# Optimization experiments

Measured on AMD Instinct MI355X. Metric: run time of the kernel, lower is better.

The kernel has to match this reference:

```python
import jax, jax.numpy as jnp
import numpy as np

BUFFER_SIZE = 64  # chunk size == sliding window size


def setup_inputs() -> dict:
    key = jax.random.key(0)
    k1, k2, k3, k4 = jax.random.split(key, 4)
    B, S, dim = 4, 8192, 256
    D = dim * 2
    states = jax.random.normal(k1, (B, S, dim, 2), dtype=jnp.float32)
    # projection weights (module inits them to identity; use scaled random for a
    # non-trivial but numerically tame reference)
    Wq = jax.random.normal(k2, (D, D), dtype=jnp.float32) * 0.05
    Wk = jax.random.normal(k3, (D, D), dtype=jnp.float32) * 0.05
    Wv = jax.random.normal(k4, (D, D), dtype=jnp.float32) * 0.05
    return {"states": states, "Wq": Wq, "Wk": Wk, "Wv": Wv}


def reference(states, Wq, Wk, Wv):
    B, S, dim, _ = states.shape
    D = dim * 2
    C = BUFFER_SIZE
    assert S % C == 0 and S > 2 * C
    n = S // C  # number of chunks

    x = states.reshape(B, S, D)
    q = x @ Wq.T
    k = x @ Wk.T
    v = x @ Wv.T

    # chunk: [B, n, C, D]
    qc = q.reshape(B, n, C, D)
    kc = k.reshape(B, n, C, D)
    vc = v.reshape(B, n, C, D)

    # context for chunk i = chunk i-1 ++ chunk i  -> [B, n, 2C, D]
    zeros_blk = jnp.zeros_like(kc[:, :1])
    k_ctx = jnp.concatenate([jnp.concatenate([zeros_blk, kc[:, :-1]], axis=1), kc], axis=2)
    v_ctx = jnp.concatenate([jnp.concatenate([zeros_blk, vc[:, :-1]], axis=1), vc], axis=2)

    scale = 1.0 / jnp.sqrt(jnp.asarray(D, dtype=q.dtype))
    scores = jnp.einsum('bnqd,bnkd->bnqk', qc, k_ctx) * scale  # [B, n, C, 2C]

    # mask: query at local pos qi attends keys strictly before it (global),
    # i.e. context index j < C + qi; chunk 0 has no previous chunk (j >= C).
    qi = jnp.arange(C)[:, None]            # [C,1]
    j = jnp.arange(2 * C)[None, :]         # [1,2C]
    chunk_idx = jnp.arange(n)[:, None, None]
    mask = (j < C + qi)[None] & ((chunk_idx > 0) | (j >= C)[None])  # [n, C, 2C]

    scores = jnp.where(mask[None], scores, jnp.asarray(-1e30, scores.dtype))
    p = jax.nn.softmax(scores, axis=-1)
    # fully-masked rows (only global position 0) -> zero output
    row_valid = jnp.any(mask, axis=-1, keepdims=True)[None].astype(p.dtype)
    p = p * row_valid

    out = jnp.einsum('bnqk,bnkd->bnqd', p, v_ctx).reshape(B, S, D)
    out = out.at[:, 0, :].set(0.0)  # matches retrieved_flat[:, 0, :] = 0.0
    return out.reshape(B, S, dim, 2)
```

## Files before the change

### kernel.cpp

```cpp
#include <hip/hip_runtime.h>

#define SCALE 0.044194173824159216f

typedef _Float16 half8 __attribute__((ext_vector_type(8)));
typedef _Float16 half4 __attribute__((ext_vector_type(4)));
typedef float    f32x4 __attribute__((ext_vector_type(4)));

#define MFMA(A, B, Cc) __builtin_amdgcn_mfma_f32_16x16x32_f16((A), (B), (Cc), 0, 0, 0)

#define X16_OFF 0ull
#define Y16_OFF 33554432ull
#define MT_OFF  67108864ull
#define MP_OFF  68157440ull
#define VT_OFF  100663296ull
#define W16_OFF 134217728ull
#define WS_NEED 135790592ull

typedef __attribute__((address_space(1))) const unsigned int glb_t;
typedef __attribute__((address_space(3))) unsigned int lds_t;

__device__ __forceinline__ void gl16(const void* g, void* l) {
  __builtin_amdgcn_global_load_lds((glb_t*)g, (lds_t*)l, 16, 0, 0);
}

__device__ __forceinline__ half8 ldf64(const _Float16* buf, int row, int colh) {
  int byte = row * 128 + (((colh) << 1) ^ ((row & 7) << 4));
  return *(const half8*)((const char*)buf + byte);
}
__device__ __forceinline__ half8 ldf128(const _Float16* buf, int row, int colh) {
  int byte = row * 256 + (((colh) << 1) ^ ((row & 7) << 4));
  return *(const half8*)((const char*)buf + byte);
}

__global__ __launch_bounds__(256)
void k0_cvt(const float* __restrict__ x, const float* __restrict__ Wq,
            const float* __restrict__ Wk, const float* __restrict__ Wv,
            _Float16* __restrict__ x16, _Float16* __restrict__ w16)
{
  const long long NX = 16777216LL;
  long long base = ((long long)blockIdx.x * 256 + threadIdx.x) * 8;
  const float* src;
  _Float16* dst;
  float sc = 1.0f;
  if (base < NX) {
    src = x + base; dst = x16 + base;
  } else {
    long long o = base - NX;
    int ws = (int)(o >> 18);
    long long oo = o & 262143LL;
    src = (ws == 0 ? Wq : (ws == 1 ? Wk : Wv)) + oo;
    dst = w16 + o;
    if (ws == 0) sc = SCALE;
  }
  const float4* p = (const float4*)src;
  float4 f0 = p[0], f1 = p[1];
  half8 v;
  v[0] = (_Float16)(f0.x * sc); v[1] = (_Float16)(f0.y * sc);
  v[2] = (_Float16)(f0.z * sc); v[3] = (_Float16)(f0.w * sc);
  v[4] = (_Float16)(f1.x * sc); v[5] = (_Float16)(f1.y * sc);
  v[6] = (_Float16)(f1.z * sc); v[7] = (_Float16)(f1.w * sc);
  *(half8*)dst = v;
}

__global__ __launch_bounds__(256)
void kmmA(const float* __restrict__ Wq, const float* __restrict__ Wk,
          float* __restrict__ part)
{
  const int blk = blockIdx.x, t = threadIdx.x;
  const int fc = blk & 7, ot = blk >> 3;
  const int G0 = (ot >> 3) * 64, E0 = (ot & 7) * 64;
  const int gb = G0 + (t & 15) * 4;
  const int eb = E0 + (t >> 4) * 4;
  float acc[4][4] = {};
  const int f0 = fc * 64;
  #pragma unroll 4
  for (int f = f0; f < f0 + 64; ++f) {
    f32x4 kv = *(const f32x4*)(Wk + (size_t)f * 512 + gb);
    f32x4 qv = *(const f32x4*)(Wq + (size_t)f * 512 + eb);
    #pragma unroll
    for (int i = 0; i < 4; ++i)
      #pragma unroll
      for (int j = 0; j < 4; ++j)
        acc[i][j] += kv[i] * qv[j];
  }
  float* pp = part + (size_t)fc * 262144;
  #pragma unroll
  for (int i = 0; i < 4; ++i)
    *(f32x4*)(pp + (size_t)(gb + i) * 512 + eb) =
        (f32x4){acc[i][0], acc[i][1], acc[i][2], acc[i][3]};
}

__global__ __launch_bounds__(256)
void kmmB(const float* __restrict__ part, _Float16* __restrict__ Mt)
{
  const int idx = blockIdx.x * 256 + threadIdx.x;
  float s = 0.f;
  #pragma unroll
  for (int fc = 0; fc < 8; ++fc)
    s += part[(size_t)fc * 262144 + idx];
  Mt[idx] = (_Float16)(s * SCALE);
}

__global__ __launch_bounds__(256)
void k1_gemm(const _Float16* __restrict__ x16, const _Float16* __restrict__ w16,
             const _Float16* __restrict__ Mt, _Float16* __restrict__ y16,
             _Float16* __restrict__ vT)
{
  __shared__ _Float16 xs[2][8192];
  __shared__ _Float16 wl[2][8192];

  const int id  = blockIdx.x;
  const int swz = (id & 7) * 256 + (id >> 3);
  const int ntile = swz & 7;
  const int stile = swz >> 3;
  const bool vpath = (ntile >= 4);
  const int tid = threadIdx.x, lane = tid & 63, w = tid >> 6;
  const int l15 = lane & 15, h = lane >> 4;
  const int wm = w >> 1, wn = w & 1;

  const _Float16* xb = x16 + (size_t)stile * 128 * 512;
  const _Float16* wb = vpath ? w16 + (size_t)(1024 + (ntile & 3) * 128) * 512
                             : Mt  + (size_t)((ntile & 3) * 128) * 512;

  int rowi[4], coli[4];
  #pragma unroll
  for (int i = 0; i < 4; ++i) {
    int unit = i * 256 + w * 64 + lane;
    int row = unit >> 3, u = unit & 7;
    rowi[i] = row;
    coli[i] = (u ^ (row & 7)) << 3;
  }

  f32x4 acc[4][4] = {};

  #pragma unroll
  for (int i = 0; i < 4; ++i) {
    int ub = i * 256 + w * 64;
    gl16(xb + (size_t)rowi[i] * 512 + coli[i], &xs[0][ub * 8]);
    gl16(wb + (size_t)rowi[i] * 512 + coli[i], &wl[0][ub * 8]);
  }

  for (int kk = 0; kk < 8; ++kk) {
    const int cur = kk & 1;
    if (kk < 7) {
      const int nxt = cur ^ 1;
      #pragma unroll
      for (int i = 0; i < 4; ++i) {
        int ub = i * 256 + w * 64;
        gl16(xb + (size_t)rowi[i] * 512 + (kk + 1) * 64 + coli[i], &xs[nxt][ub * 8]);
        gl16(wb + (size_t)rowi[i] * 512 + (kk + 1) * 64 + coli[i], &wl[nxt][ub * 8]);
      }
      asm volatile("s_waitcnt vmcnt(8)" ::: "memory");
    } else {
      asm volatile("s_waitcnt vmcnt(0)" ::: "memory");
    }
    __builtin_amdgcn_s_barrier();
    __builtin_amdgcn_sched_barrier(0);

    #pragma unroll
    for (int ks = 0; ks < 2; ++ks) {
      half8 a[4], bf[4];
      if (!vpath) {
        #pragma unroll
        for (int mr = 0; mr < 4; ++mr) a[mr]  = ldf64(xs[cur], wm * 64 + mr * 16 + l15, ks * 32 + h * 8);
        #pragma unroll
        for (int nr = 0; nr < 4; ++nr) bf[nr] = ldf64(wl[cur], wn * 64 + nr * 16 + l15, ks * 32 + h * 8);
      } else {
        #pragma unroll
        for (int mr = 0; mr < 4; ++mr) a[mr]  = ldf64(wl[cur], wm * 64 + mr * 16 + l15, ks * 32 + h * 8);
        #pragma unroll
        for (int nr = 0; nr < 4; ++nr) bf[nr] = ldf64(xs[cur], wn * 64 + nr * 16 + l15, ks * 32 + h * 8);
      }
      #pragma unroll
      for (int mr = 0; mr < 4; ++mr)
        #pragma unroll
        for (int nr = 0; nr < 4; ++nr)
          acc[mr][nr] = MFMA(a[mr], bf[nr], acc[mr][nr]);
    }

    __builtin_amdgcn_sched_barrier(0);
    __builtin_amdgcn_s_barrier();
  }

  if (!vpath) {
    const int m0 = stile * 128 + wm * 64;
    const int n0 = (ntile & 3) * 128 + wn * 64;
    #pragma unroll
    for (int mr = 0; mr < 4; ++mr)
      #pragma unroll
      for (int nr = 0; nr < 4; ++nr)
        #pragma unroll
        for (int r = 0; r < 4; ++r)
          y16[(size_t)(m0 + mr * 16 + h * 4 + r) * 512 + n0 + nr * 16 + l15] =
              (_Float16)acc[mr][nr][r];
  } else {
    const int d0 = (ntile & 3) * 128 + wm * 64;
    const int sg = stile * 128 + wn * 64;
    const int bb = sg >> 13, s0 = sg & 8191;
    _Float16* dst = vT + (size_t)bb * 512 * 8192;
    #pragma unroll
    for (int mr = 0; mr < 4; ++mr)
      #pragma unroll
      for (int nr = 0; nr < 4; ++nr)
        #pragma unroll
        for (int r = 0; r < 4; ++r)
          dst[(size_t)(d0 + mr * 16 + h * 4 + r) * 8192 + s0 + nr * 16 + l15] =
              (_Float16)acc[mr][nr][r];
  }
}

__global__ __launch_bounds__(256)
void k2_attn(const _Float16* __restrict__ y16, const _Float16* __restrict__ x16,
             const _Float16* __restrict__ vT, float* __restrict__ out)
{
  __shared__ _Float16 kj[2][128 * 64];
  __shared__ _Float16 p_lds[64 * 128];

  const int id = blockIdx.x;
  const int sz = (id & 7) * 64 + (id >> 3);
  const int b = sz >> 7, c = sz & 127;
  const int tid = threadIdx.x, lane = tid & 63, w = tid >> 6;
  const int l15 = lane & 15, h = lane >> 4;
  const int jbase = c * 64 - 64;

  const _Float16* qrow = y16 + (size_t)(b * 8192 + c * 64 + w * 16 + l15) * 512;
  half8 qa[16];
  #pragma unroll
  for (int ks = 0; ks < 16; ++ks) qa[ks] = *(const half8*)(qrow + ks * 32 + h * 8);

  const _Float16* kb = x16 + (size_t)b * 8192 * 512;
  const _Float16* vb = vT + (size_t)b * 512 * 8192;

  int srow[4], scol[4];
  #pragma unroll
  for (int i = 0; i < 4; ++i) {
    int unit = i * 256 + w * 64 + lane;
    int row = unit >> 3, u = unit & 7;
    int sj = jbase + row; if (sj < 0) sj = 0;
    srow[i] = sj;
    scol[i] = (u ^ (row & 7)) << 3;
  }
  int prow[4], pjs[4];
  #pragma unroll
  for (int i = 0; i < 4; ++i) {
    int unit = i * 256 + w * 64 + lane;
    int row = unit >> 4, u = unit & 15;
    int u2 = (u & 8) | ((u & 7) ^ (row & 7));
    int js = jbase + u2 * 8; if (js < 0) js = 0;
    prow[i] = row;
    pjs[i] = js;
  }

  f32x4 S[8] = {};
  #pragma unroll
  for (int i = 0; i < 4; ++i)
    gl16(kb + (size_t)srow[i] * 512 + scol[i], &kj[0][(i * 256 + w * 64) * 8]);

  #pragma unroll
  for (int ee = 0; ee < 8; ++ee) {
    if (ee < 7) {
      #pragma unroll
      for (int i = 0; i < 4; ++i)
        gl16(kb + (size_t)srow[i] * 512 + (ee + 1) * 64 + scol[i],
             &kj[(ee + 1) & 1][(i * 256 + w * 64) * 8]);
      asm volatile("s_waitcnt vmcnt(4)" ::: "memory");
    } else {
      asm volatile("s_waitcnt vmcnt(0)" ::: "memory");
    }
    __builtin_amdgcn_s_barrier();
    __builtin_amdgcn_sched_barrier(0);

    #pragma unroll
    for (int ks = 0; ks < 2; ++ks) {
      #pragma unroll
      for (int nt = 0; nt < 8; ++nt) {
        half8 bf = ldf64(kj[ee & 1], nt * 16 + l15, ks * 32 + h * 8);
        S[nt] = MFMA(qa[ee * 2 + ks], bf, S[nt]);
      }
    }
    __builtin_amdgcn_sched_barrier(0);
    __builtin_amdgcn_s_barrier();
  }

  #pragma unroll
  for (int i = 0; i < 4; ++i)
    gl16(vb + (size_t)prow[i] * 8192 + pjs[i], &kj[0][(i * 256 + w * 64) * 8]);

  #pragma unroll
  for (int jt = 0; jt < 8; ++jt) {
    int j = jt * 16 + l15;
    #pragma unroll
    for (int r = 0; r < 4; ++r) {
      int ql = w * 16 + h * 4 + r;
      bool valid = (j < 64 + ql) && ((c > 0) || (j >= 64));
      S[jt][r] = valid ? S[jt][r] : -1e30f;
    }
  }
  #pragma unroll
  for (int r = 0; r < 4; ++r) {
    float mx = -1e30f;
    #pragma unroll
    for (int jt = 0; jt < 8; ++jt) mx = fmaxf(mx, S[jt][r]);
    mx = fmaxf(mx, __shfl_xor(mx, 1));
    mx = fmaxf(mx, __shfl_xor(mx, 2));
    mx = fmaxf(mx, __shfl_xor(mx, 4));
    mx = fmaxf(mx, __shfl_xor(mx, 8));
    float sum = 0.f;
    #pragma unroll
    for (int jt = 0; jt < 8; ++jt) {
      float sv = S[jt][r];
      float pe = (sv > -1e29f) ? __expf(sv - mx) : 0.f;
      S[jt][r] = pe;
      sum += pe;
    }
    sum += __shfl_xor(sum, 1);
    sum += __shfl_xor(sum, 2);
    sum += __shfl_xor(sum, 4);
    sum += __shfl_xor(sum, 8);
    float inv = (sum > 0.f) ? (1.0f / sum) : 0.f;
    #pragma unroll
    for (int jt = 0; jt < 8; ++jt) {
      int row = w * 16 + h * 4 + r, col = jt * 16 + l15;
      _Float16 ph = (_Float16)(S[jt][r] * inv);
      *(_Float16*)((char*)p_lds + row * 256 + ((col << 1) ^ ((row & 7) << 4))) = ph;
    }
  }
  half8 pa[4];
  #pragma unroll
  for (int ks = 0; ks < 4; ++ks) {
    int row = w * 16 + l15, colh = ks * 32 + h * 8;
    pa[ks] = *(const half8*)((const char*)p_lds + row * 256 + ((colh << 1) ^ ((row & 7) << 4)));
  }

  float* ob = out + (size_t)(b * 8192 + c * 64 + w * 16) * 512;
  #pragma unroll
  for (int dd = 0; dd < 8; ++dd) {
    if (dd < 7) {
      #pragma unroll
      for (int i = 0; i < 4; ++i)
        gl16(vb + (size_t)((dd + 1) * 64 + prow[i]) * 8192 + pjs[i],
             &kj[(dd + 1) & 1][(i * 256 + w * 64) * 8]);
      asm volatile("s_waitcnt vmcnt(4)" ::: "memory");
    } else {
      asm volatile("s_waitcnt vmcnt(0)" ::: "memory");
    }
    __builtin_amdgcn_s_barrier();
    __builtin_amdgcn_sched_barrier(0);

    f32x4 o[4] = {};
    #pragma unroll
    for (int ks = 0; ks < 4; ++ks) {
      #pragma unroll
      for (int nr = 0; nr < 4; ++nr) {
        half8 bf = ldf128(kj[dd & 1], nr * 16 + l15, ks * 32 + h * 8);
        o[nr] = MFMA(pa[ks], bf, o[nr]);
      }
    }
    #pragma unroll
    for (int nr = 0; nr < 4; ++nr)
      #pragma unroll
      for (int r = 0; r < 4; ++r)
        ob[(size_t)(h * 4 + r) * 512 + dd * 64 + nr * 16 + l15] = o[nr][r];
    __builtin_amdgcn_sched_barrier(0);
    __builtin_amdgcn_s_barrier();
  }
}

__device__ __forceinline__ int swzb(int row, int colByte) {
  return colByte ^ ((row & 7) << 4);
}
__device__ __forceinline__ half8 ldw_frag(const float* __restrict__ W, int row, int e0) {
  const float4* p = reinterpret_cast<const float4*>(W + ((size_t)row << 9) + e0);
  float4 f0 = p[0];
  float4 f1 = p[1];
  half8 v;
  v[0] = (_Float16)f0.x; v[1] = (_Float16)f0.y; v[2] = (_Float16)f0.z; v[3] = (_Float16)f0.w;
  v[4] = (_Float16)f1.x; v[5] = (_Float16)f1.y; v[6] = (_Float16)f1.z; v[7] = (_Float16)f1.w;
  return v;
}
__device__ __forceinline__ half8 ldl_frag(const unsigned short* buf, int row, int col, int strideBytes) {
  int byte = row * strideBytes + swzb(row, col << 1);
  return *reinterpret_cast<const half8*>(reinterpret_cast<const char*>(buf) + byte);
}

__global__ __launch_bounds__(256, 1)
void ep_fused(const float* __restrict__ x, const float* __restrict__ Wq,
              const float* __restrict__ Wk, const float* __restrict__ Wv,
              float* __restrict__ out)
{
  __shared__ unsigned short xs[128 * 512];
  __shared__ unsigned short kv[64 * 128];
  __shared__ unsigned short pq[64 * 128];

  const int bc   = blockIdx.x;
  const int b    = bc >> 7;
  const int c    = bc & 127;
  const int tid  = threadIdx.x;
  const int lane = tid & 63;
  const int w    = tid >> 6;
  const int l15  = lane & 15;
  const int h    = lane >> 4;

  const float* xb = x + (size_t)b * (8192 * 512);
  #pragma unroll
  for (int i = 0; i < 32; ++i) {
    int unit = tid + (i << 8);
    int row  = unit >> 6;
    int e0   = (unit & 63) << 3;
    half8 v;
    if (c == 0 && row < 64) {
      #pragma unroll
      for (int t = 0; t < 8; ++t) v[t] = (_Float16)0.0f;
    } else {
      int s = c * 64 - 64 + row;
      const float4* p = reinterpret_cast<const float4*>(xb + (size_t)s * 512 + e0);
      float4 f0 = p[0], f1 = p[1];
      v[0] = (_Float16)f0.x; v[1] = (_Float16)f0.y; v[2] = (_Float16)f0.z; v[3] = (_Float16)f0.w;
      v[4] = (_Float16)f1.x; v[5] = (_Float16)f1.y; v[6] = (_Float16)f1.z; v[7] = (_Float16)f1.w;
    }
    int byte = (row << 10) + swzb(row, e0 << 1);
    *reinterpret_cast<half8*>(reinterpret_cast<char*>(xs) + byte) = v;
  }
  __syncthreads();

  f32x4 Sacc[8] = {};
  const int d0 = (w << 4) + (h << 2);

  for (int dt = 0; dt < 8; ++dt) {
    const int drow = (dt << 6) + (w << 4) + l15;

    f32x4 qa[4] = {};
    for (int ks = 0; ks < 16; ++ks) {
      half8 a = ldw_frag(Wq, drow, (ks << 5) + (h << 3));
      #pragma unroll
      for (int nt = 0; nt < 4; ++nt) {
        half8 bf = ldl_frag(xs, 64 + (nt << 4) + l15, (ks << 5) + (h << 3), 1024);
        qa[nt] = MFMA(a, bf, qa[nt]);
      }
    }
    #pragma unroll
    for (int nt = 0; nt < 4; ++nt) {
      int q = (nt << 4) + l15;
      half4 hv;
      hv[0] = (_Float16)qa[nt][0]; hv[1] = (_Float16)qa[nt][1];
      hv[2] = (_Float16)qa[nt][2]; hv[3] = (_Float16)qa[nt][3];
      *reinterpret_cast<half4*>(reinterpret_cast<char*>(pq) + q * 128 + swzb(q, d0 << 1)) = hv;
    }

    f32x4 ka[8] = {};
    for (int ks = 0; ks < 16; ++ks) {
      half8 a = ldw_frag(Wk, drow, (ks << 5) + (h << 3));
      #pragma unroll
      for (int nt = 0; nt < 8; ++nt) {
        half8 bf = ldl_frag(xs, (nt << 4) + l15, (ks << 5) + (h << 3), 1024);
        ka[nt] = MFMA(a, bf, ka[nt]);
      }
    }
    #pragma unroll
    for (int nt = 0; nt < 8; ++nt) {
      int j = (nt << 4) + l15;
      half4 hv;
      hv[0] = (_Float16)ka[nt][0]; hv[1] = (_Float16)ka[nt][1];
      hv[2] = (_Float16)ka[nt][2]; hv[3] = (_Float16)ka[nt][3];
      *reinterpret_cast<half4*>(reinterpret_cast<char*>(kv) + j * 128 + swzb(j, d0 << 1)) = hv;
    }
    __syncthreads();

    #pragma unroll
    for (int ksd = 0; ksd < 2; ++ksd) {
      half8 a = ldl_frag(pq, (w << 4) + l15, (ksd << 5) + (h << 3), 128);
      #pragma unroll
      for (int nt = 0; nt < 8; ++nt) {
        half8 bf = ldl_frag(kv, (nt << 4) + l15, (ksd << 5) + (h << 3), 128);
        Sacc[nt] = MFMA(a, bf, Sacc[nt]);
      }
    }
    __syncthreads();
  }

  const float scale = SCALE;
  #pragma unroll
  for (int nt = 0; nt < 8; ++nt) {
    int j = (nt << 4) + l15;
    #pragma unroll
    for (int r = 0; r < 4; ++r) {
      int qrow = (w << 4) + (h << 2) + r;
      bool valid = (j < 64 + qrow) && ((c > 0) || (j >= 64));
      Sacc[nt][r] = valid ? Sacc[nt][r] * scale : -1e30f;
    }
  }
  float inv[4];
  #pragma unroll
  for (int r = 0; r < 4; ++r) {
    float mx = -1e30f;
    #pragma unroll
    for (int nt = 0; nt < 8; ++nt) mx = fmaxf(mx, Sacc[nt][r]);
    mx = fmaxf(mx, __shfl_xor(mx, 1));
    mx = fmaxf(mx, __shfl_xor(mx, 2));
    mx = fmaxf(mx, __shfl_xor(mx, 4));
    mx = fmaxf(mx, __shfl_xor(mx, 8));
    float sum = 0.f;
    #pragma unroll
    for (int nt = 0; nt < 8; ++nt) {
      float sv = Sacc[nt][r];
      float pe = (sv > -1e29f) ? __expf(sv - mx) : 0.f;
      Sacc[nt][r] = pe;
      sum += pe;
    }
    sum += __shfl_xor(sum, 1);
    sum += __shfl_xor(sum, 2);
    sum += __shfl_xor(sum, 4);
    sum += __shfl_xor(sum, 8);
    inv[r] = (sum > 0.f) ? (1.0f / sum) : 0.f;
  }
  #pragma unroll
  for (int nt = 0; nt < 8; ++nt) {
    int j = (nt << 4) + l15;
    #pragma unroll
    for (int r = 0; r < 4; ++r) {
      int qrow = (w << 4) + (h << 2) + r;
      _Float16 ph = (_Float16)(Sacc[nt][r] * inv[r]);
      *reinterpret_cast<_Float16*>(reinterpret_cast<char*>(pq) + qrow * 256 + swzb(qrow, j << 1)) = ph;
    }
  }
  __syncthreads();

  for (int dt = 0; dt < 8; ++dt) {
    const int dcol = (dt << 6) + (w << 4) + l15;

    f32x4 va[8] = {};
    for (int ks = 0; ks < 16; ++ks) {
      half8 bf = ldw_frag(Wv, dcol, (ks << 5) + (h << 3));
      #pragma unroll
      for (int mt = 0; mt < 8; ++mt) {
        half8 a = ldl_frag(xs, (mt << 4) + l15, (ks << 5) + (h << 3), 1024);
        va[mt] = MFMA(a, bf, va[mt]);
      }
    }
    {
      int dl = (w << 4) + l15;
      #pragma unroll
      for (int mt = 0; mt < 8; ++mt) {
        int j0 = (mt << 4) + (h << 2);
        half4 hv;
        hv[0] = (_Float16)va[mt][0]; hv[1] = (_Float16)va[mt][1];
        hv[2] = (_Float16)va[mt][2]; hv[3] = (_Float16)va[mt][3];
        *reinterpret_cast<half4*>(reinterpret_cast<char*>(kv) + dl * 256 + swzb(dl, j0 << 1)) = hv;
      }
    }
    __syncthreads();

    f32x4 oa[4] = {};
    #pragma unroll
    for (int ks = 0; ks < 4; ++ks) {
      half8 a = ldl_frag(pq, (w << 4) + l15, (ks << 5) + (h << 3), 256);
      #pragma unroll
      for (int nt = 0; nt < 4; ++nt) {
        half8 bf = ldl_frag(kv, (nt << 4) + l15, (ks << 5) + (h << 3), 256);
        oa[nt] = MFMA(a, bf, oa[nt]);
      }
    }
    #pragma unroll
    for (int nt = 0; nt < 4; ++nt) {
      int d = (dt << 6) + (nt << 4) + l15;
      #pragma unroll
      for (int r = 0; r < 4; ++r) {
        int qrow = (w << 4) + (h << 2) + r;
        out[((size_t)(b * 8192 + (c << 6) + qrow) << 9) + d] = oa[nt][r];
      }
    }
    __syncthreads();
  }
}

extern "C" void kernel_launch(void* const* d_in, const int* in_sizes, int n_in,
                              void* d_out, int out_size, void* d_ws, size_t ws_size,
                              hipStream_t stream) {
  const float* x  = (const float*)d_in[0];
  const float* Wq = (const float*)d_in[1];
  const float* Wk = (const float*)d_in[2];
  const float* Wv = (const float*)d_in[3];
  float* out = (float*)d_out;
  (void)in_sizes; (void)n_in; (void)out_size;

  if (d_ws != nullptr && ws_size >= WS_NEED) {
    char* ws = (char*)d_ws;
    _Float16* x16 = (_Float16*)(ws + X16_OFF);
    _Float16* y16 = (_Float16*)(ws + Y16_OFF);
    _Float16* Mt  = (_Float16*)(ws + MT_OFF);
    float*    Mp  = (float*)(ws + MP_OFF);
    _Float16* vT  = (_Float16*)(ws + VT_OFF);
    _Float16* w16 = (_Float16*)(ws + W16_OFF);

    hipLaunchKernelGGL(kmmA, dim3(512), dim3(256), 0, stream, Wq, Wk, Mp);
    hipLaunchKernelGGL(k0_cvt, dim3(8576), dim3(256), 0, stream, x, Wq, Wk, Wv, x16, w16);
    hipLaunchKernelGGL(kmmB, dim3(1024), dim3(256), 0, stream, Mp, Mt);
    hipLaunchKernelGGL(k1_gemm, dim3(2048), dim3(256), 0, stream, x16, w16, Mt, y16, vT);
    hipLaunchKernelGGL(k2_attn, dim3(512), dim3(256), 0, stream, y16, x16, vT, out);
  } else {
    hipLaunchKernelGGL(ep_fused, dim3(512), dim3(256), 0, stream, x, Wq, Wk, Wv, out);
  }
}
```

Before: 103.7 us.

## Pre-pack weight operands into MFMA fragment layout and load them directly to registers

```diff
diff --git a/kernel.cpp b/kernel.cpp
--- a/kernel.cpp
+++ b/kernel.cpp
@@ -12,6 +12,7 @@
 #define Y16_OFF 33554432ull
 #define MT_OFF  67108864ull
 #define MP_OFF  68157440ull
+#define WF_OFF  76546048ull
 #define VT_OFF  100663296ull
 #define W16_OFF 134217728ull
 #define WS_NEED 135790592ull
@@ -91,23 +92,43 @@
 }
 
 __global__ __launch_bounds__(256)
-void kmmB(const float* __restrict__ part, _Float16* __restrict__ Mt)
+void kmmB(const float* __restrict__ part, const _Float16* __restrict__ w16,
+          _Float16* __restrict__ wfrag)
 {
-  const int idx = blockIdx.x * 256 + threadIdx.x;
-  float s = 0.f;
-  #pragma unroll
-  for (int fc = 0; fc < 8; ++fc)
-    s += part[(size_t)fc * 262144 + idx];
-  Mt[idx] = (_Float16)(s * SCALE);
+  const int T = blockIdx.x * 256 + threadIdx.x;
+  const int lane = T & 63;
+  const int rbi  = (T >> 6) & 7;
+  const int ks   = (T >> 9) & 1;
+  const int kk   = (T >> 10) & 7;
+  const int ntile = T >> 13;
+  const int gl = rbi * 16 + (lane & 15);
+  const int e0 = kk * 64 + ks * 32 + (lane >> 4) * 8;
+  half8 v;
+  if (ntile < 4) {
+    const int g = ntile * 128 + gl;
+    float s[8] = {};
+    #pragma unroll
+    for (int fc = 0; fc < 8; ++fc) {
+      const float* pp = part + (size_t)fc * 262144 + (size_t)g * 512 + e0;
+      f32x4 a = *(const f32x4*)pp;
+      f32x4 b = *(const f32x4*)(pp + 4);
+      s[0] += a[0]; s[1] += a[1]; s[2] += a[2]; s[3] += a[3];
+      s[4] += b[0]; s[5] += b[1]; s[6] += b[2]; s[7] += b[3];
+    }
+    #pragma unroll
+    for (int j = 0; j < 8; ++j) v[j] = (_Float16)(s[j] * SCALE);
+  } else {
+    const int g = (ntile - 4) * 128 + gl;
+    v = *(const half8*)(w16 + (size_t)(1024 + g) * 512 + e0);
+  }
+  *(half8*)(wfrag + (size_t)T * 8) = v;
 }
 
 __global__ __launch_bounds__(256)
-void k1_gemm(const _Float16* __restrict__ x16, const _Float16* __restrict__ w16,
-             const _Float16* __restrict__ Mt, _Float16* __restrict__ y16,
-             _Float16* __restrict__ vT)
+void k1_gemm(const _Float16* __restrict__ x16, const _Float16* __restrict__ wfrag,
+             _Float16* __restrict__ y16, _Float16* __restrict__ vT)
 {
   __shared__ _Float16 xs[2][8192];
-  __shared__ _Float16 wl[2][8192];
 
   const int id  = blockIdx.x;
   const int swz = (id & 7) * 256 + (id >> 3);
@@ -119,8 +140,8 @@
   const int wm = w >> 1, wn = w & 1;
 
   const _Float16* xb = x16 + (size_t)stile * 128 * 512;
-  const _Float16* wb = vpath ? w16 + (size_t)(1024 + (ntile & 3) * 128) * 512
-                             : Mt  + (size_t)((ntile & 3) * 128) * 512;
+  const int rbsel = vpath ? wm : wn;
+  const _Float16* wfb = wfrag + (size_t)ntile * 65536 + (size_t)rbsel * 4 * 512 + lane * 8;
 
   int rowi[4], coli[4];
   #pragma unroll
@@ -132,25 +153,31 @@
   }
 
   f32x4 acc[4][4] = {};
-
-  #pragma unroll
-  for (int i = 0; i < 4; ++i) {
-    int ub = i * 256 + w * 64;
-    gl16(xb + (size_t)rowi[i] * 512 + coli[i], &xs[0][ub * 8]);
-    gl16(wb + (size_t)rowi[i] * 512 + coli[i], &wl[0][ub * 8]);
-  }
+  half8 wf[2][8];
+
+  #pragma unroll
+  for (int i = 0; i < 4; ++i)
+    gl16(xb + (size_t)rowi[i] * 512 + coli[i], &xs[0][(i * 256 + w * 64) * 8]);
+  #pragma unroll
+  for (int f = 0; f < 4; ++f)
+    #pragma unroll
+    for (int ks = 0; ks < 2; ++ks)
+      wf[0][f * 2 + ks] = *(const half8*)(wfb + ((0 * 2 + ks) * 8 + f) * 512);
 
   for (int kk = 0; kk < 8; ++kk) {
-    const int cur = kk & 1;
+    const int cur = kk & 1, nxt = cur ^ 1;
     if (kk < 7) {
-      const int nxt = cur ^ 1;
-      #pragma unroll
-      for (int i = 0; i < 4; ++i) {
-        int ub = i * 256 + w * 64;
-        gl16(xb + (size_t)rowi[i] * 512 + (kk + 1) * 64 + coli[i], &xs[nxt][ub * 8]);
-        gl16(wb + (size_t)rowi[i] * 512 + (kk + 1) * 64 + coli[i], &wl[nxt][ub * 8]);
-      }
-      asm volatile("s_waitcnt vmcnt(8)" ::: "memory");
+      #pragma unroll
+      for (int i = 0; i < 4; ++i)
+        gl16(xb + (size_t)rowi[i] * 512 + (kk + 1) * 64 + coli[i],
+             &xs[nxt][(i * 256 + w * 64) * 8]);
+      #pragma unroll
+      for (int f = 0; f < 4; ++f)
+        #pragma unroll
+        for (int ks = 0; ks < 2; ++ks)
+          wf[nxt][f * 2 + ks] = *(const half8*)(wfb + (((kk + 1) * 2 + ks) * 8 + f) * 512);
+      __builtin_amdgcn_sched_barrier(0);
+      asm volatile("s_waitcnt vmcnt(12)" ::: "memory");
     } else {
       asm volatile("s_waitcnt vmcnt(0)" ::: "memory");
     }
@@ -159,23 +186,16 @@
 
     #pragma unroll
     for (int ks = 0; ks < 2; ++ks) {
-      half8 a[4], bf[4];
-      if (!vpath) {
-        #pragma unroll
-        for (int mr = 0; mr < 4; ++mr) a[mr]  = ldf64(xs[cur], wm * 64 + mr * 16 + l15, ks * 32 + h * 8);
-        #pragma unroll
-        for (int nr = 0; nr < 4; ++nr) bf[nr] = ldf64(wl[cur], wn * 64 + nr * 16 + l15, ks * 32 + h * 8);
-      } else {
-        #pragma unroll
-        for (int mr = 0; mr < 4; ++mr) a[mr]  = ldf64(wl[cur], wm * 64 + mr * 16 + l15, ks * 32 + h * 8);
-        #pragma unroll
-        for (int nr = 0; nr < 4; ++nr) bf[nr] = ldf64(xs[cur], wn * 64 + nr * 16 + l15, ks * 32 + h * 8);
-      }
+      half8 xf[4];
+      #pragma unroll
+      for (int f = 0; f < 4; ++f)
+        xf[f] = ldf64(xs[cur], (vpath ? wn : wm) * 64 + f * 16 + l15, ks * 32 + h * 8);
       #pragma unroll
       for (int mr = 0; mr < 4; ++mr)
         #pragma unroll
         for (int nr = 0; nr < 4; ++nr)
-          acc[mr][nr] = MFMA(a[mr], bf[nr], acc[mr][nr]);
+          acc[mr][nr] = vpath ? MFMA(wf[cur][mr * 2 + ks], xf[nr], acc[mr][nr])
+                              : MFMA(xf[mr], wf[cur][nr * 2 + ks], acc[mr][nr]);
     }
 
     __builtin_amdgcn_sched_barrier(0);
@@ -184,7 +204,7 @@
 
   if (!vpath) {
     const int m0 = stile * 128 + wm * 64;
-    const int n0 = (ntile & 3) * 128 + wn * 64;
+    const int n0 = ntile * 128 + wn * 64;
     #pragma unroll
     for (int mr = 0; mr < 4; ++mr)
       #pragma unroll
@@ -587,15 +607,15 @@
     char* ws = (char*)d_ws;
     _Float16* x16 = (_Float16*)(ws + X16_OFF);
     _Float16* y16 = (_Float16*)(ws + Y16_OFF);
-    _Float16* Mt  = (_Float16*)(ws + MT_OFF);
     float*    Mp  = (float*)(ws + MP_OFF);
+    _Float16* wf  = (_Float16*)(ws + WF_OFF);
     _Float16* vT  = (_Float16*)(ws + VT_OFF);
     _Float16* w16 = (_Float16*)(ws + W16_OFF);
 
     hipLaunchKernelGGL(kmmA, dim3(512), dim3(256), 0, stream, Wq, Wk, Mp);
     hipLaunchKernelGGL(k0_cvt, dim3(8576), dim3(256), 0, stream, x, Wq, Wk, Wv, x16, w16);
-    hipLaunchKernelGGL(kmmB, dim3(1024), dim3(256), 0, stream, Mp, Mt);
-    hipLaunchKernelGGL(k1_gemm, dim3(2048), dim3(256), 0, stream, x16, w16, Mt, y16, vT);
+    hipLaunchKernelGGL(kmmB, dim3(256), dim3(256), 0, stream, Mp, w16, wf);
+    hipLaunchKernelGGL(k1_gemm, dim3(2048), dim3(256), 0, stream, x16, wf, y16, vT);
     hipLaunchKernelGGL(k2_attn, dim3(512), dim3(256), 0, stream, y16, x16, vT, out);
   } else {
     hipLaunchKernelGGL(ep_fused, dim3(512), dim3(256), 0, stream, x, Wq, Wk, Wv, out);
```

New measurement: 338.7 us. 3.26x slower.

## Merge weight-product and conversion kernels; single-buffer weight tile in GEMM

Applied to the files above, without the earlier changes.

```diff
diff --git a/kernel.cpp b/kernel.cpp
--- a/kernel.cpp
+++ b/kernel.cpp
@@ -33,61 +33,59 @@
 }
 
 __global__ __launch_bounds__(256)
-void k0_cvt(const float* __restrict__ x, const float* __restrict__ Wq,
-            const float* __restrict__ Wk, const float* __restrict__ Wv,
-            _Float16* __restrict__ x16, _Float16* __restrict__ w16)
+void k0m(const float* __restrict__ x, const float* __restrict__ Wq,
+         const float* __restrict__ Wk, const float* __restrict__ Wv,
+         _Float16* __restrict__ x16, _Float16* __restrict__ w16,
+         float* __restrict__ part)
 {
-  const long long NX = 16777216LL;
-  long long base = ((long long)blockIdx.x * 256 + threadIdx.x) * 8;
-  const float* src;
-  _Float16* dst;
-  float sc = 1.0f;
-  if (base < NX) {
-    src = x + base; dst = x16 + base;
+  if (blockIdx.x < 512) {
+    const int blk = blockIdx.x, t = threadIdx.x;
+    const int fc = blk & 7, ot = blk >> 3;
+    const int G0 = (ot >> 3) * 64, E0 = (ot & 7) * 64;
+    const int gb = G0 + (t & 15) * 4;
+    const int eb = E0 + (t >> 4) * 4;
+    float acc[4][4] = {};
+    const int f0 = fc * 64;
+    #pragma unroll 4
+    for (int f = f0; f < f0 + 64; ++f) {
+      f32x4 kv = *(const f32x4*)(Wk + (size_t)f * 512 + gb);
+      f32x4 qv = *(const f32x4*)(Wq + (size_t)f * 512 + eb);
+      #pragma unroll
+      for (int i = 0; i < 4; ++i)
+        #pragma unroll
+        for (int j = 0; j < 4; ++j)
+          acc[i][j] += kv[i] * qv[j];
+    }
+    float* pp = part + (size_t)fc * 262144;
+    #pragma unroll
+    for (int i = 0; i < 4; ++i)
+      *(f32x4*)(pp + (size_t)(gb + i) * 512 + eb) =
+          (f32x4){acc[i][0], acc[i][1], acc[i][2], acc[i][3]};
   } else {
-    long long o = base - NX;
-    int ws = (int)(o >> 18);
-    long long oo = o & 262143LL;
-    src = (ws == 0 ? Wq : (ws == 1 ? Wk : Wv)) + oo;
-    dst = w16 + o;
-    if (ws == 0) sc = SCALE;
-  }
-  const float4* p = (const float4*)src;
-  float4 f0 = p[0], f1 = p[1];
-  half8 v;
-  v[0] = (_Float16)(f0.x * sc); v[1] = (_Float16)(f0.y * sc);
-  v[2] = (_Float16)(f0.z * sc); v[3] = (_Float16)(f0.w * sc);
-  v[4] = (_Float16)(f1.x * sc); v[5] = (_Float16)(f1.y * sc);
-  v[6] = (_Float16)(f1.z * sc); v[7] = (_Float16)(f1.w * sc);
-  *(half8*)dst = v;
-}
-
-__global__ __launch_bounds__(256)
-void kmmA(const float* __restrict__ Wq, const float* __restrict__ Wk,
-          float* __restrict__ part)
-{
-  const int blk = blockIdx.x, t = threadIdx.x;
-  const int fc = blk & 7, ot = blk >> 3;
-  const int G0 = (ot >> 3) * 64, E0 = (ot & 7) * 64;
-  const int gb = G0 + (t & 15) * 4;
-  const int eb = E0 + (t >> 4) * 4;
-  float acc[4][4] = {};
-  const int f0 = fc * 64;
-  #pragma unroll 4
-  for (int f = f0; f < f0 + 64; ++f) {
-    f32x4 kv = *(const f32x4*)(Wk + (size_t)f * 512 + gb);
-    f32x4 qv = *(const f32x4*)(Wq + (size_t)f * 512 + eb);
-    #pragma unroll
-    for (int i = 0; i < 4; ++i)
-      #pragma unroll
-      for (int j = 0; j < 4; ++j)
-        acc[i][j] += kv[i] * qv[j];
-  }
-  float* pp = part + (size_t)fc * 262144;
-  #pragma unroll
-  for (int i = 0; i < 4; ++i)
-    *(f32x4*)(pp + (size_t)(gb + i) * 512 + eb) =
-        (f32x4){acc[i][0], acc[i][1], acc[i][2], acc[i][3]};
+    const long long NX = 16777216LL;
+    long long base = ((long long)(blockIdx.x - 512) * 256 + threadIdx.x) * 8;
+    const float* src;
+    _Float16* dst;
+    float sc = 1.0f;
+    if (base < NX) {
+      src = x + base; dst = x16 + base;
+    } else {
+      long long o = base - NX;
+      int ws = (int)(o >> 18);
+      long long oo = o & 262143LL;
+      src = (ws == 0 ? Wq : (ws == 1 ? Wk : Wv)) + oo;
+      dst = w16 + o;
+      if (ws == 0) sc = SCALE;
+    }
+    const float4* p = (const float4*)src;
+    float4 f0 = p[0], f1 = p[1];
+    half8 v;
+    v[0] = (_Float16)(f0.x * sc); v[1] = (_Float16)(f0.y * sc);
+    v[2] = (_Float16)(f0.z * sc); v[3] = (_Float16)(f0.w * sc);
+    v[4] = (_Float16)(f1.x * sc); v[5] = (_Float16)(f1.y * sc);
+    v[6] = (_Float16)(f1.z * sc); v[7] = (_Float16)(f1.w * sc);
+    *(half8*)dst = v;
+  }
 }
 
 __global__ __launch_bounds__(256)
@@ -107,7 +105,7 @@
              _Float16* __restrict__ vT)
 {
   __shared__ _Float16 xs[2][8192];
-  __shared__ _Float16 wl[2][8192];
+  __shared__ _Float16 wl[8192];
 
   const int id  = blockIdx.x;
   const int swz = (id & 7) * 256 + (id >> 3);
@@ -134,23 +132,21 @@
   f32x4 acc[4][4] = {};
 
   #pragma unroll
-  for (int i = 0; i < 4; ++i) {
-    int ub = i * 256 + w * 64;
-    gl16(xb + (size_t)rowi[i] * 512 + coli[i], &xs[0][ub * 8]);
-    gl16(wb + (size_t)rowi[i] * 512 + coli[i], &wl[0][ub * 8]);
-  }
+  for (int i = 0; i < 4; ++i)
+    gl16(xb + (size_t)rowi[i] * 512 + coli[i], &xs[0][(i * 256 + w * 64) * 8]);
+  #pragma unroll
+  for (int i = 0; i < 4; ++i)
+    gl16(wb + (size_t)rowi[i] * 512 + coli[i], &wl[(i * 256 + w * 64) * 8]);
 
   for (int kk = 0; kk < 8; ++kk) {
     const int cur = kk & 1;
     if (kk < 7) {
       const int nxt = cur ^ 1;
       #pragma unroll
-      for (int i = 0; i < 4; ++i) {
-        int ub = i * 256 + w * 64;
-        gl16(xb + (size_t)rowi[i] * 512 + (kk + 1) * 64 + coli[i], &xs[nxt][ub * 8]);
-        gl16(wb + (size_t)rowi[i] * 512 + (kk + 1) * 64 + coli[i], &wl[nxt][ub * 8]);
-      }
-      asm volatile("s_waitcnt vmcnt(8)" ::: "memory");
+      for (int i = 0; i < 4; ++i)
+        gl16(xb + (size_t)rowi[i] * 512 + (kk + 1) * 64 + coli[i],
+             &xs[nxt][(i * 256 + w * 64) * 8]);
+      asm volatile("s_waitcnt vmcnt(4)" ::: "memory");
     } else {
       asm volatile("s_waitcnt vmcnt(0)" ::: "memory");
     }
@@ -164,10 +160,10 @@
         #pragma unroll
         for (int mr = 0; mr < 4; ++mr) a[mr]  = ldf64(xs[cur], wm * 64 + mr * 16 + l15, ks * 32 + h * 8);
         #pragma unroll
-        for (int nr = 0; nr < 4; ++nr) bf[nr] = ldf64(wl[cur], wn * 64 + nr * 16 + l15, ks * 32 + h * 8);
+        for (int nr = 0; nr < 4; ++nr) bf[nr] = ldf64(wl, wn * 64 + nr * 16 + l15, ks * 32 + h * 8);
       } else {
         #pragma unroll
-        for (int mr = 0; mr < 4; ++mr) a[mr]  = ldf64(wl[cur], wm * 64 + mr * 16 + l15, ks * 32 + h * 8);
+        for (int mr = 0; mr < 4; ++mr) a[mr]  = ldf64(wl, wm * 64 + mr * 16 + l15, ks * 32 + h * 8);
         #pragma unroll
         for (int nr = 0; nr < 4; ++nr) bf[nr] = ldf64(xs[cur], wn * 64 + nr * 16 + l15, ks * 32 + h * 8);
       }
@@ -180,6 +176,12 @@
 
     __builtin_amdgcn_sched_barrier(0);
     __builtin_amdgcn_s_barrier();
+    if (kk < 7) {
+      #pragma unroll
+      for (int i = 0; i < 4; ++i)
+        gl16(wb + (size_t)rowi[i] * 512 + (kk + 1) * 64 + coli[i],
+             &wl[(i * 256 + w * 64) * 8]);
+    }
   }
 
   if (!vpath) {
@@ -592,8 +594,7 @@
     _Float16* vT  = (_Float16*)(ws + VT_OFF);
     _Float16* w16 = (_Float16*)(ws + W16_OFF);
 
-    hipLaunchKernelGGL(kmmA, dim3(512), dim3(256), 0, stream, Wq, Wk, Mp);
-    hipLaunchKernelGGL(k0_cvt, dim3(8576), dim3(256), 0, stream, x, Wq, Wk, Wv, x16, w16);
+    hipLaunchKernelGGL(k0m, dim3(9088), dim3(256), 0, stream, x, Wq, Wk, Wv, x16, w16, Mp);
     hipLaunchKernelGGL(kmmB, dim3(1024), dim3(256), 0, stream, Mp, Mt);
     hipLaunchKernelGGL(k1_gemm, dim3(2048), dim3(256), 0, stream, x16, w16, Mt, y16, vT);
     hipLaunchKernelGGL(k2_attn, dim3(512), dim3(256), 0, stream, y16, x16, vT, out);
```

After: 99.02 us. 4.6% less time.
